# Kernel optimization log

Measured on AMD Instinct MI355X. Metric: run time of the kernel, lower is better.

The kernel has to match this reference:

```python
import jax, jax.numpy as jnp
import numpy as np

HEADS = 4
PATCH = 32
KSIZE = 5


def conv2d(x, w, groups=1):
    return jax.lax.conv_general_dilated(
        x, w, (1, 1), 'SAME', feature_group_count=groups,
        dimension_numbers=('NCHW', 'OIHW', 'NCHW'))


def window_starts(size, step, d):
    return [min(i, size - d) for i in range(0, size + step - d, step)]


def local_partition(x, tops, lefts, dh, dw):
    wins = [x[:, :, t:t + dh, l:l + dw] for t in tops for l in lefts]
    return jnp.stack(wins, axis=1)  # (b, nwin, c, dh, dw)


def local_reverse(local_x, shape, tops, lefts, dh, dw):
    b, c, h, w = shape
    out = jnp.zeros(shape, local_x.dtype)
    cnt = jnp.zeros((h, w), local_x.dtype)
    idx = 0
    for t in tops:
        for l in lefts:
            out = out.at[:, :, t:t + dh, l:l + dw].add(local_x[:, idx])
            cnt = cnt.at[t:t + dh, l:l + dw].add(1.0)
            idx += 1
    out = out / cnt  # broadcast over (b, c)
    return jnp.nan_to_num(out, nan=1e-5, posinf=1e-5, neginf=1e-5)


def dynamic_filtering(x, w1, w2, ks):
    # x: (b, c, t, h, w); conv3d kernels have size 1 in t -> per-frame 2D conv
    b, c, t, h, w = x.shape
    y = x.transpose(0, 2, 1, 3, 4).reshape(b * t, c, h, w)
    f = conv2d(y, w1)
    f = jnp.where(f >= 0, f, 0.2 * f)  # LeakyReLU(0.2)
    ker = conv2d(f, w2).reshape(b, t, ks * ks, h, w)
    K = t * ks * ks
    # rearrange 'b (k1 k2) t h w -> b h w (t k1 k2)' then normalize over last dim
    kerf = ker.transpose(0, 3, 4, 1, 2).reshape(b, h, w, K)
    kerf = kerf - jnp.mean(kerf, axis=-1, keepdims=True) + 1.0 / K
    kern = kerf.reshape(b, h, w, t, ks * ks).transpose(0, 3, 4, 1, 2)  # (b,t,kk,h,w)
    p = (ks - 1) // 2
    xp = jnp.pad(x, ((0, 0), (0, 0), (0, 0), (p, p), (p, p)), mode='edge')
    out = jnp.zeros((b, c, h, w), x.dtype)
    for ti in range(t):  # small fixed loops (t*ks*ks taps) instead of full unfold
        for kk in range(ks * ks):
            di, dj = kk // ks, kk % ks
            out = out + xp[:, :, ti, di:di + h, dj:dj + w] * kern[:, ti, kk][:, None]
    return out


def forward(x, k_cached, v_cached, W_qkv, W_dw, W_f1, W_f2, W_proj, temperature):
    b, c, h, w = x.shape
    ph = pw = PATCH
    qkv = jnp.einsum('oc,bchw->bohw', W_qkv, x)          # 1x1 conv
    qkv = conv2d(qkv, W_dw, groups=3 * c)                 # 3x3 depthwise
    q, k, v = jnp.split(qkv, 3, axis=1)
    k_ = jnp.concatenate([k_cached, k[:, :, None]], axis=2)
    v_ = jnp.concatenate([v_cached, k[:, :, None]], axis=2)  # faithful to source (uses k, not v)
    k = dynamic_filtering(k_, W_f1, W_f2, KSIZE)
    v = dynamic_filtering(v_, W_f1, W_f2, KSIZE)
    tops = window_starts(h, h - ph // 4, ph)
    lefts = window_starts(w, w - pw // 4, pw)
    nwin = len(tops) * len(lefts)
    ch = c // HEADS

    def split_heads(t):
        loc = local_partition(t, tops, lefts, ph, pw)  # (b,nwin,c,ph,pw)
        return loc.reshape(b * nwin, HEADS, ch, ph * pw).transpose(0, 1, 3, 2)

    qh, kh, vh = split_heads(q), split_heads(k), split_heads(v)
    qh = qh / jnp.maximum(jnp.linalg.norm(qh, axis=-1, keepdims=True), 1e-12)
    kh = kh / jnp.maximum(jnp.linalg.norm(kh, axis=-1, keepdims=True), 1e-12)
    attn = jnp.einsum('nhsc,nhtc->nhst', qh, kh) * temperature  # temperature (H,1,1)
    attn = jax.nn.softmax(attn, axis=-1)
    oh = jnp.einsum('nhst,nhtc->nhsc', attn, vh)
    loc = oh.transpose(0, 1, 3, 2).reshape(b, nwin, c, ph, pw)
    out = local_reverse(loc, (b, c, h, w), tops, lefts, ph, pw)
    out = jnp.einsum('oc,bchw->bohw', W_proj, out)        # 1x1 conv
    return out, k_[:, :, -2:], v_[:, :, -2:]


def setup_inputs() -> dict:
    key = jax.random.key(0)
    ks = jax.random.split(key, 8)
    d = 64
    return {
        'x': jax.random.normal(ks[0], (8, d, 64, 64), jnp.float32),
        'k_cached': jax.random.normal(ks[1], (8, d, 1, 64, 64), jnp.float32),
        'v_cached': jax.random.normal(ks[2], (8, d, 1, 64, 64), jnp.float32),
        'W_qkv': 0.05 * jax.random.normal(ks[3], (3 * d, d), jnp.float32),
        'W_dw': 0.05 * jax.random.normal(ks[4], (3 * d, 1, 3, 3), jnp.float32),
        'W_f1': 0.05 * jax.random.normal(ks[5], (d, d, 3, 3), jnp.float32),
        'W_f2': 0.05 * jax.random.normal(ks[6], (KSIZE * KSIZE, d, 3, 3), jnp.float32),
        'W_proj': 0.05 * jax.random.normal(ks[7], (d, d), jnp.float32),
        'temperature': jnp.ones((HEADS, 1, 1), jnp.float32),
    }


def reference(x, k_cached, v_cached, W_qkv, W_dw, W_f1, W_f2, W_proj, temperature):
    return forward(x, k_cached, v_cached, W_qkv, W_dw, W_f1, W_f2, W_proj, temperature)
```

## Files before the change

### kernel.cpp

```cpp
#include <hip/hip_runtime.h>
#include <math.h>

#define B_ 8
#define C_ 64
#define HW_ 4096

#define OUT_N   2097152
#define KV_N    4194304

typedef short s4v __attribute__((ext_vector_type(4)));
typedef short s8v __attribute__((ext_vector_type(8)));
typedef float f4v __attribute__((ext_vector_type(4)));
typedef unsigned int u2v __attribute__((ext_vector_type(2)));
typedef unsigned short ushort_t;

__device__ inline unsigned short f2bf(float f) {
    unsigned int u = __builtin_bit_cast(unsigned int, f);
    u += 0x7FFFu + ((u >> 16) & 1u);
    return (unsigned short)(u >> 16);
}

__device__ inline unsigned int bfpack_t(float a, float b) {
    unsigned int ua = __builtin_bit_cast(unsigned int, a);
    unsigned int ub = __builtin_bit_cast(unsigned int, b);
    return __builtin_amdgcn_perm(ub, ua, 0x07060302u);
}

#define MFMA16(a, b, c) __builtin_amdgcn_mfma_f32_16x16x16bf16_1k(a, b, c, 0, 0, 0)
#define LO4(v) __builtin_shufflevector(v, v, 0, 1, 2, 3)
#define HI4(v) __builtin_shufflevector(v, v, 4, 5, 6, 7)

__global__ __launch_bounds__(256) void k0_copy(const float4* __restrict__ kc,
                                               const float4* __restrict__ vc,
                                               float* __restrict__ k_out,
                                               float* __restrict__ v_out) {
    int i = blockIdx.x * 256 + threadIdx.x;
    const int n4 = (B_ * C_ * HW_) / 4;
    int which = (i >= n4);
    int j = which ? i - n4 : i;
    const float4* src = which ? vc : kc;
    float4 v = src[j];
    int bc = j >> 10, hw4 = j & 1023;
    float* dst = (which ? v_out : k_out) + ((size_t)bc * 2) * HW_ + hw4 * 4;
    *(float4*)dst = v;
}

__global__ __launch_bounds__(256) void wprep(const float* __restrict__ Wf1,
                                             const float* __restrict__ Wf2,
                                             ushort_t* __restrict__ wt1,
                                             ushort_t* __restrict__ wt2) {
    int id = blockIdx.x * 256 + threadIdx.x;
    if (id >= 6912) return;
    ushort_t o[8];
    if (id < 4608) {
        int lane = id & 63; int p = (id >> 6) % 18; int ocg = id / (18 * 64);
        int tap = p >> 1, m = p & 1;
        int oc = ocg * 16 + (lane & 15);
        int ic0 = m * 32 + (lane >> 4) * 8;
#pragma unroll
        for (int j = 0; j < 8; ++j)
            o[j] = f2bf(Wf1[((size_t)oc * 64 + ic0 + j) * 9 + tap]);
        *(uint4*)(wt1 + (size_t)id * 8) = *(uint4*)o;
    } else {
        int id2 = id - 4608;
        int lane = id2 & 63; int p = (id2 >> 6) % 18; int ocg = id2 / (18 * 64);
        int tap = p >> 1, m = p & 1;
        int oc = ocg * 16 + (lane & 15);
        int ic0 = m * 32 + (lane >> 4) * 8;
#pragma unroll
        for (int j = 0; j < 8; ++j)
            o[j] = (oc < 25) ? f2bf(Wf2[((size_t)oc * 64 + ic0 + j) * 9 + tap]) : (ushort_t)0;
        *(uint4*)(wt2 + (size_t)id2 * 8) = *(uint4*)o;
    }
}

__global__ __launch_bounds__(256) void k1_mfma(const float* __restrict__ x,
                                               const float* __restrict__ Wqkv,
                                               float* __restrict__ qkv) {
    int blk = blockIdx.x;
    int tid = threadIdx.x, lane = tid & 63, wv = tid >> 6;
    int px0 = (blk & 15) * 256 + wv * 64;
    int otile = (blk >> 4) & 7, b = blk >> 7;
    int ln15 = lane & 15, g4 = (lane >> 4) * 4;

    const float* xb = x + (size_t)b * 64 * HW_;
    s4v wf[4];
#pragma unroll
    for (int k = 0; k < 4; ++k) {
        const float* wr = Wqkv + (size_t)(otile * 16 + ln15) * 64 + k * 16 + g4;
        float4 w4 = *(const float4*)wr;
        u2v u; u.x = bfpack_t(w4.x, w4.y); u.y = bfpack_t(w4.z, w4.w);
        wf[k] = __builtin_bit_cast(s4v, u);
    }
    const f4v zf = {0.f, 0.f, 0.f, 0.f};
    f4v acc[4] = {zf, zf, zf, zf};
#pragma unroll
    for (int k = 0; k < 4; ++k) {
#pragma unroll
        for (int p = 0; p < 4; ++p) {
            const float* xp = xb + (size_t)(k * 16 + g4) * HW_ + px0 + p * 16 + ln15;
            float v0 = xp[0];
            float v1 = xp[HW_];
            float v2 = xp[2 * HW_];
            float v3 = xp[3 * HW_];
            u2v u; u.x = bfpack_t(v0, v1); u.y = bfpack_t(v2, v3);
            s4v xf = __builtin_bit_cast(s4v, u);
            acc[p] = MFMA16(wf[k], xf, acc[p]);
        }
    }
    float* ob = qkv + ((size_t)b * 128 + otile * 16) * HW_ + px0;
#pragma unroll
    for (int p = 0; p < 4; ++p)
#pragma unroll
        for (int j = 0; j < 4; ++j)
            ob[(size_t)(g4 + j) * HW_ + p * 16 + ln15] = acc[p][j];
}

__global__ __launch_bounds__(256) void k2_dw(const float* __restrict__ qkv,
                                             const float* __restrict__ Wdw,
                                             float* __restrict__ qbuf,
                                             float* __restrict__ k_out,
                                             float* __restrict__ v_out) {
    int t = blockIdx.x * 256 + threadIdx.x;
    int hw = t & 4095; int bo = t >> 12; int o = bo & 127; int b = bo >> 7;
    int y = hw >> 6, xx0 = hw & 63;
    const float* in = qkv + (size_t)bo * HW_;
    const float* w = Wdw + o * 9;
    float acc = 0.f;
#pragma unroll
    for (int dy = 0; dy < 3; ++dy) {
        int yy = y + dy - 1;
        if (yy < 0 || yy > 63) continue;
#pragma unroll
        for (int dx = 0; dx < 3; ++dx) {
            int xx = xx0 + dx - 1;
            if (xx < 0 || xx > 63) continue;
            acc = fmaf(in[yy * 64 + xx], w[dy * 3 + dx], acc);
        }
    }
    if (o < 64) {
        qbuf[((size_t)b * 64 + o) * HW_ + hw] = acc;
    } else {
        int oc = o - 64;
        size_t off = (((size_t)b * 64 + oc) * 2 + 1) * HW_ + hw;
        k_out[off] = acc;
        v_out[off] = acc;
    }
}

__global__ __launch_bounds__(256) void k3_mfma1(const float* __restrict__ k_out,
                                                const float* __restrict__ vc,
                                                const ushort_t* __restrict__ wt1,
                                                ushort_t* __restrict__ fb16) {
    int stripe = blockIdx.x;
    int f = blockIdx.y;
    int tid = threadIdx.x;
    __shared__ ushort_t ilds[4 * 66 * 72];
    const float* src; size_t icstr;
    if (f < 16) { src = k_out + (((size_t)(f >> 1) * 128) + (f & 1)) * HW_; icstr = 2 * HW_; }
    else        { src = vc + ((size_t)(f - 16) * 64) * HW_;                 icstr = HW_; }
    int y0 = stripe * 2;

    int lane = tid & 63, wv = tid >> 6, g = lane >> 4, c16 = lane & 15;
    s8v a[18];
    const ushort_t* wb = wt1 + ((size_t)wv * 18) * 512 + lane * 8;
#pragma unroll
    for (int p = 0; p < 18; ++p) a[p] = *(const s8v*)(wb + p * 512);

    {
        int rc = tid >> 5, idx = tid & 31;
        int r = rc >> 1, side = rc & 1;
        ((unsigned int*)ilds)[(r * 66 + side * 65) * 36 + idx] = 0u;
    }
    {
        int r = tid >> 6, x = tid & 63;
        int y = y0 - 1 + r;
        bool valid = (y >= 0 && y < 64);
        const float* rowp = src + y * 64 + x;
        ushort_t* dst = ilds + ((r * 66) + x + 1) * 72;
#pragma unroll
        for (int ic4 = 0; ic4 < 16; ++ic4) {
            ushort_t o[4];
#pragma unroll
            for (int j = 0; j < 4; ++j) {
                float v = valid ? rowp[(size_t)(ic4 * 4 + j) * icstr] : 0.f;
                o[j] = f2bf(v);
            }
            *(uint2*)(dst + ic4 * 4) = *(uint2*)o;
        }
    }
    __syncthreads();

#pragma unroll
    for (int r_out = 0; r_out < 2; ++r_out)
#pragma unroll
        for (int xp = 0; xp < 2; ++xp) {
            int x0 = xp * 32, x1 = x0 + 16;
            f4v acc0 = {0.f, 0.f, 0.f, 0.f}, acc1 = {0.f, 0.f, 0.f, 0.f};
#pragma unroll
            for (int tap = 0; tap < 9; ++tap) {
                const int dy = tap / 3, dx = tap % 3;
                const ushort_t* bp0 = ilds + (((r_out + dy) * 66) + x0 + c16 + dx) * 72 + g * 8;
                const ushort_t* bp1 = ilds + (((r_out + dy) * 66) + x1 + c16 + dx) * 72 + g * 8;
                s8v b00 = *(const s8v*)bp0;
                s8v b01 = *(const s8v*)(bp0 + 32);
                s8v b10 = *(const s8v*)bp1;
                s8v b11 = *(const s8v*)(bp1 + 32);
                acc0 = MFMA16(LO4(a[2 * tap]),     LO4(b00), acc0);
                acc1 = MFMA16(LO4(a[2 * tap]),     LO4(b10), acc1);
                acc0 = MFMA16(HI4(a[2 * tap]),     HI4(b00), acc0);
                acc1 = MFMA16(HI4(a[2 * tap]),     HI4(b10), acc1);
                acc0 = MFMA16(LO4(a[2 * tap + 1]), LO4(b01), acc0);
                acc1 = MFMA16(LO4(a[2 * tap + 1]), LO4(b11), acc1);
                acc0 = MFMA16(HI4(a[2 * tap + 1]), HI4(b01), acc0);
                acc1 = MFMA16(HI4(a[2 * tap + 1]), HI4(b11), acc1);
            }
            int py = (y0 + r_out) * 64;
#pragma unroll
            for (int j = 0; j < 4; ++j) {
                int oc = wv * 16 + g * 4 + j;
                float v0 = acc0[j]; v0 = (v0 >= 0.f) ? v0 : 0.2f * v0;
                float v1 = acc1[j]; v1 = (v1 >= 0.f) ? v1 : 0.2f * v1;
                fb16[((size_t)f * 64 + oc) * HW_ + py + x0 + c16] = f2bf(v0);
                fb16[((size_t)f * 64 + oc) * HW_ + py + x1 + c16] = f2bf(v1);
            }
        }
}

__global__ __launch_bounds__(256) void k3b_mfma2(const ushort_t* __restrict__ fb16,
                                                 const ushort_t* __restrict__ wt2,
                                                 float* __restrict__ kerb) {
    int stripe = blockIdx.x;
    int f = blockIdx.y;
    int tid = threadIdx.x;
    __shared__ ushort_t ilds[4 * 66 * 72];
    int y0 = stripe * 2;

    int lane = tid & 63, wv = tid >> 6, g = lane >> 4, c16 = lane & 15;
    int ocg = wv & 1, xh = wv >> 1;
    s8v a[18];
    const ushort_t* wb = wt2 + ((size_t)ocg * 18) * 512 + lane * 8;
#pragma unroll
    for (int p = 0; p < 18; ++p) a[p] = *(const s8v*)(wb + p * 512);

    {
        int rc = tid >> 5, idx = tid & 31;
        int r = rc >> 1, side = rc & 1;
        ((unsigned int*)ilds)[(r * 66 + side * 65) * 36 + idx] = 0u;
    }
    {
        int r = tid >> 6, x = tid & 63;
        int y = y0 - 1 + r;
        bool valid = (y >= 0 && y < 64);
        const ushort_t* rowp = fb16 + (size_t)f * 64 * HW_ + y * 64 + x;
        ushort_t* dst = ilds + ((r * 66) + x + 1) * 72;
#pragma unroll
        for (int ic4 = 0; ic4 < 16; ++ic4) {
            ushort_t o[4];
#pragma unroll
            for (int j = 0; j < 4; ++j)
                o[j] = valid ? rowp[(size_t)(ic4 * 4 + j) * HW_] : (ushort_t)0;
            *(uint2*)(dst + ic4 * 4) = *(uint2*)o;
        }
    }
    __syncthreads();

#pragma unroll
    for (int r_out = 0; r_out < 2; ++r_out) {
        int x0 = xh * 32, x1 = x0 + 16;
        f4v acc0 = {0.f, 0.f, 0.f, 0.f}, acc1 = {0.f, 0.f, 0.f, 0.f};
#pragma unroll
        for (int tap = 0; tap < 9; ++tap) {
            const int dy = tap / 3, dx = tap % 3;
            const ushort_t* bp0 = ilds + (((r_out + dy) * 66) + x0 + c16 + dx) * 72 + g * 8;
            const ushort_t* bp1 = ilds + (((r_out + dy) * 66) + x1 + c16 + dx) * 72 + g * 8;
            s8v b00 = *(const s8v*)bp0;
            s8v b01 = *(const s8v*)(bp0 + 32);
            s8v b10 = *(const s8v*)bp1;
            s8v b11 = *(const s8v*)(bp1 + 32);
            acc0 = MFMA16(LO4(a[2 * tap]),     LO4(b00), acc0);
            acc1 = MFMA16(LO4(a[2 * tap]),     LO4(b10), acc1);
            acc0 = MFMA16(HI4(a[2 * tap]),     HI4(b00), acc0);
            acc1 = MFMA16(HI4(a[2 * tap]),     HI4(b10), acc1);
            acc0 = MFMA16(LO4(a[2 * tap + 1]), LO4(b01), acc0);
            acc1 = MFMA16(LO4(a[2 * tap + 1]), LO4(b11), acc1);
            acc0 = MFMA16(HI4(a[2 * tap + 1]), HI4(b01), acc0);
            acc1 = MFMA16(HI4(a[2 * tap + 1]), HI4(b11), acc1);
        }
        int py = (y0 + r_out) * 64;
#pragma unroll
        for (int j = 0; j < 4; ++j) {
            int oc = ocg * 16 + g * 4 + j;
            if (oc < 25) {
                kerb[((size_t)f * 25 + oc) * HW_ + py + x0 + c16] = acc0[j];
                kerb[((size_t)f * 25 + oc) * HW_ + py + x1 + c16] = acc1[j];
            }
        }
    }
}

__global__ __launch_bounds__(256) void k4b_apply(const float* __restrict__ kerb,
                                                 const float* __restrict__ k_out,
                                                 const float* __restrict__ v_out,
                                                 float* __restrict__ kfil,
                                                 float* __restrict__ vfil) {
    int y = blockIdx.x, b = blockIdx.y;
    int p = blockIdx.z >> 1, chh = blockIdx.z & 1;
    int tid = threadIdx.x;
    __shared__ float klds[50][64];
    __shared__ float part[4][64];
    int f0 = (p == 0) ? 2 * b : 16 + b;
    int f1 = 2 * b + 1;
    for (int idx = tid; idx < 3200; idx += 256) {
        int px_ = idx & 63, j = idx >> 6;
        int ti = (j >= 25); int kk = j - ti * 25;
        int fr = ti ? f1 : f0;
        klds[j][px_] = kerb[((size_t)fr * 25 + kk) * HW_ + y * 64 + px_];
    }
    __syncthreads();
    {
        int px_ = tid & 63, q_ = tid >> 6;
        int j0 = q_ * 13; int j1 = j0 + 13; if (j1 > 50) j1 = 50;
        float s = 0.f;
        for (int j = j0; j < j1; ++j) s += klds[j][px_];
        part[q_][px_] = s;
    }
    __syncthreads();
    if (tid < 64) {
        float m = (part[0][tid] + part[1][tid]) + (part[2][tid] + part[3][tid]);
        part[0][tid] = m * (1.f / 50.f);
    }
    __syncthreads();
    for (int idx = tid; idx < 3200; idx += 256) {
        int px_ = idx & 63, j = idx >> 6;
        klds[j][px_] += 0.02f - part[0][px_];
    }
    __syncthreads();

    int px = tid & 63, cq = tid >> 6;
    const float* xsrc = ((p == 0) ? k_out : v_out)
                      + (size_t)b * 64 * 2 * HW_ + (size_t)chh * 32 * 2 * HW_;
    float acc[8];
#pragma unroll
    for (int i = 0; i < 8; ++i) acc[i] = 0.f;

#pragma unroll
    for (int ti = 0; ti < 2; ++ti) {
        for (int kk = 0; kk < 25; ++kk) {
            int cy = y + kk / 5 - 2;  cy = cy < 0 ? 0 : (cy > 63 ? 63 : cy);
            int cx = px + kk % 5 - 2; cx = cx < 0 ? 0 : (cx > 63 ? 63 : cx);
            float kv = klds[ti * 25 + kk][px];
            const float* xb = xsrc + (size_t)ti * HW_ + cy * 64 + cx;
#pragma unroll
            for (int i = 0; i < 8; ++i)
                acc[i] = fmaf(xb[(size_t)(cq + 4 * i) * 2 * HW_], kv, acc[i]);
        }
    }
    float* ob = ((p == 0) ? kfil : vfil)
              + ((size_t)b * 64 + chh * 32) * HW_ + y * 64 + px;
#pragma unroll
    for (int i = 0; i < 8; ++i) ob[(size_t)(cq + 4 * i) * HW_] = acc[i];
}

__global__ __launch_bounds__(256) void k4c_cvt(const float* __restrict__ qbuf,
                                               const float* __restrict__ kfil,
                                               unsigned short* __restrict__ qbf,
                                               unsigned short* __restrict__ kbf) {
    int row = blockIdx.x * 256 + threadIdx.x;
    int unit = blockIdx.y;
    int which = blockIdx.z;
    int win = unit & 3, head = (unit >> 2) & 3, b = unit >> 4;
    int wy = win >> 1, wx = win & 1;
    int gpx = ((wy * 32 + (row >> 5)) << 6) + wx * 32 + (row & 31);
    const float* src = (which ? kfil : qbuf) + ((size_t)b * 64 + head * 16) * HW_ + gpx;
    float v[16]; float ss = 0.f;
#pragma unroll
    for (int i = 0; i < 16; ++i) { v[i] = src[(size_t)i * HW_]; ss = fmaf(v[i], v[i], ss); }
    float sc = 1.f / fmaxf(sqrtf(ss), 1e-12f);
    unsigned short o[16];
#pragma unroll
    for (int i = 0; i < 16; ++i) o[i] = f2bf(v[i] * sc);
    unsigned short* dst = (which ? kbf : qbf) + ((size_t)unit * 1024 + row) * 16;
    ((uint4*)dst)[0] = ((uint4*)o)[0];
    ((uint4*)dst)[1] = ((uint4*)o)[1];
}

__global__ __launch_bounds__(256) void k5_mfma(const unsigned short* __restrict__ qbf,
                                               const unsigned short* __restrict__ kbf,
                                               const float* __restrict__ vfil,
                                               const float* __restrict__ temp,
                                               float* __restrict__ attno) {
    int qb = blockIdx.x;
    int unit = blockIdx.y;
    int win = unit & 3, head = (unit >> 2) & 3, b = unit >> 4;
    int wy = win >> 1, wx = win & 1;
    int tid = threadIdx.x, lane = tid & 63, wv = tid >> 6;
    __shared__ unsigned short vt[16][1032];
    size_t cbase = ((size_t)b * 64 + head * 16) * HW_;

#pragma unroll
    for (int it = 0; it < 4; ++it) {
        int i = it * 256 + tid;
        int ch = i >> 6, k16 = (i & 63) << 4;
        int gpx = ((wy * 32 + (k16 >> 5)) << 6) + wx * 32 + (k16 & 31);
        const float* src = vfil + cbase + (size_t)ch * HW_ + gpx;
        unsigned int w[8];
#pragma unroll
        for (int j = 0; j < 8; ++j) w[j] = bfpack_t(src[2 * j], src[2 * j + 1]);
        uint4* d = (uint4*)&vt[ch][k16];
        d[0] = *(uint4*)&w[0];
        d[1] = *(uint4*)&w[4];
    }

    float tmp = temp[head];
    float a_s = tmp * 1.44269504f;
    float b_s = (fabsf(tmp) + 1e-6f) * 1.44269504f;

    int ln15 = lane & 15, g4 = (lane >> 4) * 4;
    const unsigned short* qu = qbf + (size_t)unit * 1024 * 16;
    const unsigned short* ku = kbf + (size_t)unit * 1024 * 16;
    int qt0 = qb * 8 + wv * 2;
    s4v qf0 = *(const s4v*)(qu + ((size_t)(qt0 * 16 + ln15)) * 16 + g4);
    s4v qf1 = *(const s4v*)(qu + ((size_t)((qt0 + 1) * 16 + ln15)) * 16 + g4);

    const short one_bf = (short)0x3F80;
    const s4v ones = {one_bf, one_bf, one_bf, one_bf};
    const f4v zf = {0.f, 0.f, 0.f, 0.f};
    f4v o0 = zf, o1 = zf, lacc0 = zf, lacc1 = zf;

    __syncthreads();
#pragma unroll 4
    for (int tb = 0; tb < 64; ++tb) {
        s4v kf = *(const s4v*)(ku + ((size_t)(tb * 16 + ln15)) * 16 + g4);
        s4v vf = *(const s4v*)(&vt[ln15][tb * 16 + g4]);
        f4v s0 = MFMA16(kf, qf0, zf);
        f4v s1 = MFMA16(kf, qf1, zf);
        float p00 = __builtin_amdgcn_exp2f(fmaf(s0[0], a_s, -b_s));
        float p01 = __builtin_amdgcn_exp2f(fmaf(s0[1], a_s, -b_s));
        float p02 = __builtin_amdgcn_exp2f(fmaf(s0[2], a_s, -b_s));
        float p03 = __builtin_amdgcn_exp2f(fmaf(s0[3], a_s, -b_s));
        float p10 = __builtin_amdgcn_exp2f(fmaf(s1[0], a_s, -b_s));
        float p11 = __builtin_amdgcn_exp2f(fmaf(s1[1], a_s, -b_s));
        float p12 = __builtin_amdgcn_exp2f(fmaf(s1[2], a_s, -b_s));
        float p13 = __builtin_amdgcn_exp2f(fmaf(s1[3], a_s, -b_s));
        u2v u0; u0.x = bfpack_t(p00, p01); u0.y = bfpack_t(p02, p03);
        u2v u1; u1.x = bfpack_t(p10, p11); u1.y = bfpack_t(p12, p13);
        s4v pf0 = __builtin_bit_cast(s4v, u0);
        s4v pf1 = __builtin_bit_cast(s4v, u1);
        o0 = MFMA16(vf, pf0, o0);
        o1 = MFMA16(vf, pf1, o1);
        lacc0 = MFMA16(ones, pf0, lacc0);
        lacc1 = MFMA16(ones, pf1, lacc1);
    }

    float inv0 = 1.f / lacc0[0], inv1 = 1.f / lacc1[0];

    int q0 = qt0 * 16 + ln15;
    int q1 = q0 + 16;
    int gq0 = ((wy * 32 + (q0 >> 5)) << 6) + wx * 32 + (q0 & 31);
    int gq1 = ((wy * 32 + (q1 >> 5)) << 6) + wx * 32 + (q1 & 31);
#pragma unroll
    for (int j = 0; j < 4; ++j) {
        attno[cbase + (size_t)(g4 + j) * HW_ + gq0] = o0[j] * inv0;
        attno[cbase + (size_t)(g4 + j) * HW_ + gq1] = o1[j] * inv1;
    }
}

__global__ __launch_bounds__(256) void k6_mfma(const float* __restrict__ attno,
                                               const float* __restrict__ Wp,
                                               float* __restrict__ out) {
    int blk = blockIdx.x;
    int tid = threadIdx.x, lane = tid & 63, wv = tid >> 6;
    int px0 = (blk & 15) * 256 + wv * 64;
    int otile = (blk >> 4) & 3, b = blk >> 6;
    int ln15 = lane & 15, g4 = (lane >> 4) * 4;

    const float* ab = attno + (size_t)b * 64 * HW_;
    s4v wf[4];
#pragma unroll
    for (int k = 0; k < 4; ++k) {
        const float* wr = Wp + (size_t)(otile * 16 + ln15) * 64 + k * 16 + g4;
        float4 w4 = *(const float4*)wr;
        u2v u; u.x = bfpack_t(w4.x, w4.y); u.y = bfpack_t(w4.z, w4.w);
        wf[k] = __builtin_bit_cast(s4v, u);
    }
    const f4v zf = {0.f, 0.f, 0.f, 0.f};
    f4v acc[4] = {zf, zf, zf, zf};
#pragma unroll
    for (int k = 0; k < 4; ++k) {
#pragma unroll
        for (int p = 0; p < 4; ++p) {
            const float* xp = ab + (size_t)(k * 16 + g4) * HW_ + px0 + p * 16 + ln15;
            float v0 = xp[0];
            float v1 = xp[HW_];
            float v2 = xp[2 * HW_];
            float v3 = xp[3 * HW_];
            u2v u; u.x = bfpack_t(v0, v1); u.y = bfpack_t(v2, v3);
            s4v xf = __builtin_bit_cast(s4v, u);
            acc[p] = MFMA16(wf[k], xf, acc[p]);
        }
    }
    float* ob = out + ((size_t)b * 64 + otile * 16) * HW_ + px0;
#pragma unroll
    for (int p = 0; p < 4; ++p)
#pragma unroll
        for (int j = 0; j < 4; ++j)
            ob[(size_t)(g4 + j) * HW_ + p * 16 + ln15] = acc[p][j];
}

extern "C" void kernel_launch(void* const* d_in, const int* in_sizes, int n_in,
                              void* d_out, int out_size, void* d_ws, size_t ws_size,
                              hipStream_t stream) {
    const float* x    = (const float*)d_in[0];
    const float* kc   = (const float*)d_in[1];
    const float* vc   = (const float*)d_in[2];
    const float* Wqkv = (const float*)d_in[3];
    const float* Wdw  = (const float*)d_in[4];
    const float* Wf1  = (const float*)d_in[5];
    const float* Wf2  = (const float*)d_in[6];
    const float* Wpr  = (const float*)d_in[7];
    const float* temp = (const float*)d_in[8];

    float* out   = (float*)d_out;
    float* k_out = out + OUT_N;
    float* v_out = out + OUT_N + KV_N;

    float* ws   = (float*)d_ws;
    float* qkv  = ws;
    unsigned short* fb16 = (unsigned short*)ws;
    unsigned short* qbf = (unsigned short*)ws;
    unsigned short* kbf = (unsigned short*)(ws + 1048576);
    float* qbuf = ws + 6291456;
    float* kerb = ws + 8388608;
    float* kfil = ws + 10846208;
    float* vfil = ws + 12943360;
    unsigned short* wt1 = (unsigned short*)(ws + 15106048);
    unsigned short* wt2 = wt1 + 36864;
    float* attno= kerb;

    wprep   <<<27,    256, 0, stream>>>(Wf1, Wf2, wt1, wt2);
    k0_copy <<<4096,  256, 0, stream>>>((const float4*)kc, (const float4*)vc, k_out, v_out);
    k1_mfma <<<1024,  256, 0, stream>>>(x, Wqkv, qkv);
    k2_dw   <<<16384, 256, 0, stream>>>(qkv, Wdw, qbuf, k_out, v_out);
    k3_mfma1<<<dim3(32, 24), 256, 0, stream>>>(k_out, vc, wt1, fb16);
    k3b_mfma2<<<dim3(32, 24), 256, 0, stream>>>(fb16, wt2, kerb);
    k4b_apply<<<dim3(64, 8, 4), 256, 0, stream>>>(kerb, k_out, v_out, kfil, vfil);
    k4c_cvt <<<dim3(4, 128, 2), 256, 0, stream>>>(qbuf, kfil, qbf, kbf);
    k5_mfma <<<dim3(8, 128), 256, 0, stream>>>(qbf, kbf, vfil, temp, attno);
    k6_mfma <<<512,   256, 0, stream>>>(attno, Wpr, out);
}
```

Baseline: 173.1 us.

## Stage clamped input rows in LDS for dynamic filter apply and split channels finer

The dynamic-filter apply kernel now loads a 5-row, edge-clamped halo tile of 16 channels into shared memory for each time step, then computes the 25 taps from LDS instead of doing repeated clamped global loads. Each block handles 16 channels rather than 32, so the grid doubles and each thread accumulates 4 channels instead of 8. This removes redundant global/cache traffic from the overlapping 5x5 window reads. In exchange it adds about 21 KB of LDS per block, extra barriers, and recomputes the per-pixel kernel normalization in twice as many blocks.

After: 207.7 us, median of 3. 20.0% more time.

```diff
diff --git a/kernel.cpp b/kernel.cpp
--- a/kernel.cpp
+++ b/kernel.cpp
@@ -305,10 +305,11 @@
                                                  float* __restrict__ kfil,
                                                  float* __restrict__ vfil) {
     int y = blockIdx.x, b = blockIdx.y;
-    int p = blockIdx.z >> 1, chh = blockIdx.z & 1;
+    int p = blockIdx.z >> 2, cq4 = blockIdx.z & 3;
     int tid = threadIdx.x;
     __shared__ float klds[50][64];
     __shared__ float part[4][64];
+    __shared__ float xl[5 * 16 * 68];
     int f0 = (p == 0) ? 2 * b : 16 + b;
     int f1 = 2 * b + 1;
     for (int idx = tid; idx < 3200; idx += 256) {
@@ -335,31 +336,38 @@
         int px_ = idx & 63, j = idx >> 6;
         klds[j][px_] += 0.02f - part[0][px_];
     }
-    __syncthreads();
-
-    int px = tid & 63, cq = tid >> 6;
+
+    int px = tid & 63, cg = tid >> 6;
     const float* xsrc = ((p == 0) ? k_out : v_out)
-                      + (size_t)b * 64 * 2 * HW_ + (size_t)chh * 32 * 2 * HW_;
-    float acc[8];
-#pragma unroll
-    for (int i = 0; i < 8; ++i) acc[i] = 0.f;
-
-#pragma unroll
+                      + ((size_t)b * 64 + cq4 * 16) * 2 * HW_;
+    float acc[4] = {0.f, 0.f, 0.f, 0.f};
+
     for (int ti = 0; ti < 2; ++ti) {
-        for (int kk = 0; kk < 25; ++kk) {
-            int cy = y + kk / 5 - 2;  cy = cy < 0 ? 0 : (cy > 63 ? 63 : cy);
-            int cx = px + kk % 5 - 2; cx = cx < 0 ? 0 : (cx > 63 ? 63 : cx);
-            float kv = klds[ti * 25 + kk][px];
-            const float* xb = xsrc + (size_t)ti * HW_ + cy * 64 + cx;
-#pragma unroll
-            for (int i = 0; i < 8; ++i)
-                acc[i] = fmaf(xb[(size_t)(cq + 4 * i) * 2 * HW_], kv, acc[i]);
+        __syncthreads();
+        for (int e = tid; e < 5440; e += 256) {
+            int r = e / 1088, rem = e - r * 1088;
+            int ch = rem / 68, px2 = rem - ch * 68;
+            int sy = y - 2 + r; sy = sy < 0 ? 0 : (sy > 63 ? 63 : sy);
+            int sx = px2 - 2;   sx = sx < 0 ? 0 : (sx > 63 ? 63 : sx);
+            xl[e] = xsrc[((size_t)ch * 2 + ti) * HW_ + sy * 64 + sx];
+        }
+        __syncthreads();
+#pragma unroll
+        for (int r = 0; r < 5; ++r) {
+#pragma unroll
+            for (int dx = 0; dx < 5; ++dx) {
+                float kv = klds[ti * 25 + r * 5 + dx][px];
+                const float* xp = xl + (r * 16 + cg * 4) * 68 + px + dx;
+#pragma unroll
+                for (int i = 0; i < 4; ++i)
+                    acc[i] = fmaf(xp[i * 68], kv, acc[i]);
+            }
         }
     }
     float* ob = ((p == 0) ? kfil : vfil)
-              + ((size_t)b * 64 + chh * 32) * HW_ + y * 64 + px;
-#pragma unroll
-    for (int i = 0; i < 8; ++i) ob[(size_t)(cq + 4 * i) * HW_] = acc[i];
+              + ((size_t)b * 64 + cq4 * 16 + cg * 4) * HW_ + y * 64 + px;
+#pragma unroll
+    for (int i = 0; i < 4; ++i) ob[(size_t)i * HW_] = acc[i];
 }
 
 __global__ __launch_bounds__(256) void k4c_cvt(const float* __restrict__ qbuf,
@@ -544,7 +552,7 @@
     k2_dw   <<<16384, 256, 0, stream>>>(qkv, Wdw, qbuf, k_out, v_out);
     k3_mfma1<<<dim3(32, 24), 256, 0, stream>>>(k_out, vc, wt1, fb16);
     k3b_mfma2<<<dim3(32, 24), 256, 0, stream>>>(fb16, wt2, kerb);
-    k4b_apply<<<dim3(64, 8, 4), 256, 0, stream>>>(kerb, k_out, v_out, kfil, vfil);
+    k4b_apply<<<dim3(64, 8, 8), 256, 0, stream>>>(kerb, k_out, v_out, kfil, vfil);
     k4c_cvt <<<dim3(4, 128, 2), 256, 0, stream>>>(qbuf, kfil, qbf, kbf);
     k5_mfma <<<dim3(8, 128), 256, 0, stream>>>(qbf, kbf, vfil, temp, attno);
     k6_mfma <<<512,   256, 0, stream>>>(attno, Wpr, out);
```
